# Optimization experiments

Hardware: AMD Instinct MI355X
Metric: run time of the kernel (lower is better)

The kernel has to match this reference:

```python
import jax, jax.numpy as jnp
import numpy as np

N = 100000   # every_node
IN = 128     # in_channels
OUT = 128    # out_channels
R = 8        # every_relation
B = 4        # num_bases
E = 1_600_000  # total edges (avg degree 16)
E_PER = E // R
LEAKY_SLOPE = 0.2


def _xavier_uniform(key, shape, gain):
    fan_in, fan_out = shape[-2], shape[-1]
    bound = gain * np.sqrt(6.0 / (fan_in + fan_out))
    return jax.random.uniform(key, shape, jnp.float32, -bound, bound)


def setup_inputs() -> dict:
    key = jax.random.key(0)
    k = jax.random.split(key, 6)
    gain = float(np.sqrt(2.0))  # calculate_gain('relu')
    node_embeddings = jax.random.normal(k[0], (N, IN), jnp.float32)
    src = jax.random.randint(k[1], (E,), 0, N, jnp.int32)
    dst = jax.random.randint(k[2], (E,), 0, N, jnp.int32)
    rel = jnp.repeat(jnp.arange(R, dtype=jnp.int32), E_PER)  # sorted by relation
    triples = jnp.stack([src, rel, dst], axis=1)  # [E,3] = (src, rel, dst)
    change_points = jnp.arange(0, E + 1, E_PER, dtype=jnp.int32)  # [R+1]
    basis = _xavier_uniform(k[3], (B, IN, OUT), gain)
    att = _xavier_uniform(k[4], (R, B), gain)
    attention = _xavier_uniform(k[5], (R, 2 * OUT), gain)
    bias = jnp.zeros((OUT,), jnp.float32)
    return {
        'node_embeddings': node_embeddings,
        'triples': triples,
        'change_points': change_points,
        'basis': basis,
        'att': att,
        'attention': attention,
        'bias': bias,
    }


def reference(node_embeddings, triples, change_points, basis, att, attention, bias):
    # Basis decomposition: per-relation weight, then per-relation transformed features.
    weights = jnp.einsum('rb,bio->rio', att, basis)              # [R, in, out]
    Wh = jnp.einsum('rio,ni->rno', weights, node_embeddings)     # [R, N, out]

    src, rel, dst = triples[:, 0], triples[:, 2], None  # placeholder; see below
    src = triples[:, 0]
    rel = triples[:, 1]   # triples are sorted by relation; rel column == block id from change_points
    dst = triples[:, 2]

    # Attention score a . [Wh_src || Wh_dst] decomposed into per-node partial scores.
    a_src = attention[:, :OUT]                                   # [R, out]
    a_dst = attention[:, OUT:]                                   # [R, out]
    s_src = jnp.einsum('rno,ro->rn', Wh, a_src)                  # [R, N]
    s_dst = jnp.einsum('rno,ro->rn', Wh, a_dst)                  # [R, N]
    e_raw = jax.nn.leaky_relu(s_src[rel, src] + s_dst[rel, dst], LEAKY_SLOPE)  # [E]

    # Segment softmax per (relation, dst) — matches per-relation scatter amax/add.
    seg = rel.astype(jnp.int32) * N + dst.astype(jnp.int32)
    e_max = jax.ops.segment_max(e_raw, seg, num_segments=R * N)
    e_exp = jnp.exp(e_raw - e_max[seg])
    denom = jax.ops.segment_sum(e_exp, seg, num_segments=R * N)
    alpha = e_exp / jnp.maximum(denom[seg], 1e-8)                # [E]
    # (attn dropout omitted: eval mode)

    # SpMM aggregation: sum over relations of A_rel @ Wh_rel.
    msgs = alpha[:, None] * Wh[rel, src]                         # [E, out]
    h_prime = jax.ops.segment_sum(msgs, dst, num_segments=N)     # [N, out]

    output = h_prime + bias
    if node_embeddings.shape[-1] == OUT:
        output = output + node_embeddings  # residual
    return output
```

## Files before the change

kernel.cpp:

```cpp
#include <hip/hip_runtime.h>
#include <stdint.h>

#define NN 100000
#define DIM 128
#define RR 8
#define BB 4
#define EE 1600000
#define EPR 200000
#define SLOPE 0.2f
#define CAP 64
#define NCONV 12500
#define NBG 12504
#define NBE 6250

typedef __attribute__((ext_vector_type(8))) short short8;
typedef __attribute__((ext_vector_type(4))) float f32x4;

__device__ __forceinline__ unsigned short f2bf(float f) {
    unsigned u = __float_as_uint(f);
    unsigned r = (u + 0x7FFFu + ((u >> 16) & 1u)) >> 16;
    return (unsigned short)r;
}

__global__ __launch_bounds__(256) void k_pre(const float* __restrict__ x,
        unsigned* __restrict__ xb, int* __restrict__ cnt,
        const float* __restrict__ att, const float* __restrict__ basis,
        const float* __restrict__ attention, unsigned short* __restrict__ wt,
        unsigned short* __restrict__ w16b) {
    int bid = blockIdx.x;
    if (bid < NCONV) {
        size_t t = (size_t)bid * 256 + threadIdx.x;
        float4 v = *(const float4*)(x + t * 4);
        uint2 o;
        o.x = (unsigned)f2bf(v.x) | ((unsigned)f2bf(v.y) << 16);
        o.y = (unsigned)f2bf(v.z) | ((unsigned)f2bf(v.w) << 16);
        *(uint2*)(xb + t * 2) = o;
        if (t < NN) cnt[t] = 0;
    } else {
        int r = bid - NCONV;
        int i = threadIdx.x;
        if (i < DIM) {
            float a[BB];
#pragma unroll
            for (int b = 0; b < BB; ++b) a[b] = att[r * BB + b];
            const float* asrc = attention + r * 2 * DIM;
            const float* adst = asrc + DIM;
            float ws = 0.f, wd = 0.f;
            for (int o = 0; o < DIM; ++o) {
                float w = 0.f;
#pragma unroll
                for (int b = 0; b < BB; ++b) w += a[b] * basis[(b * DIM + i) * DIM + o];
                wt[(r * DIM + o) * DIM + i] = f2bf(w);
                ws += w * asrc[o];
                wd += w * adst[o];
            }
            w16b[r * DIM + i] = f2bf(ws);
            w16b[(RR + r) * DIM + i] = f2bf(wd);
        }
    }
}

__global__ __launch_bounds__(256) void k_score16(const unsigned short* __restrict__ w16b,
        const unsigned short* __restrict__ xb, float* __restrict__ ssrc,
        float* __restrict__ sdst) {
    __shared__ unsigned short lw[16 * 136];
    for (int u = threadIdx.x; u < 16 * 16; u += 256) {
        int row = u >> 4, ch = u & 15;
        *(uint4*)&lw[row * 136 + ch * 8] = *(const uint4*)&w16b[row * 128 + ch * 8];
    }
    __syncthreads();
    int wave = threadIdx.x >> 6, lane = threadIdx.x & 63;
    int ncol = blockIdx.x * 64 + wave * 16 + (lane & 15);
    int nc = ncol < NN ? ncol : NN - 1;
    int kg = (lane >> 4) * 8;
    const short8* xrow = (const short8*)(xb + (size_t)nc * DIM);
    f32x4 acc = (f32x4){0.f, 0.f, 0.f, 0.f};
#pragma unroll
    for (int k = 0; k < 4; ++k) {
        short8 a = *(const short8*)&lw[(lane & 15) * 136 + k * 32 + kg];
        short8 b = xrow[k * 4 + (lane >> 4)];
        acc = __builtin_amdgcn_mfma_f32_16x16x32_bf16(a, b, acc, 0, 0, 0);
    }
    if (ncol < NN) {
#pragma unroll
        for (int j = 0; j < 4; ++j) {
            int row = (lane >> 4) * 4 + j;
            if (row < RR) ssrc[row * NN + ncol] = acc[j];
            else sdst[(row - RR) * NN + ncol] = acc[j];
        }
    }
}

__global__ __launch_bounds__(256) void k_main(const unsigned short* __restrict__ wt,
        const unsigned short* __restrict__ xb, unsigned short* __restrict__ wh,
        const int* __restrict__ tri, const float* __restrict__ ssrc,
        const float* __restrict__ sdst, int* __restrict__ cnt,
        unsigned* __restrict__ bucket) {
    __shared__ unsigned short lds[DIM * 136];
    int bid = blockIdx.x;
    if (bid < NBG) {
        int r = bid & 7;
        int ncol0 = (bid >> 3) * 64;
        {
            const uint4* src = (const uint4*)(wt + r * DIM * DIM);
            for (int u = threadIdx.x; u < DIM * DIM / 8; u += 256) {
                int row = u >> 4, ch = u & 15;
                *(uint4*)&lds[row * 136 + ch * 8] = src[u];
            }
        }
        __syncthreads();
        int wave = threadIdx.x >> 6, lane = threadIdx.x & 63;
        int ncol = ncol0 + wave * 16 + (lane & 15);
        int kg = (lane >> 4) * 8;
        int nc = ncol < NN ? ncol : NN - 1;
        const short8* xrow = (const short8*)(xb + (size_t)nc * DIM);
        short8 bfrag[4];
#pragma unroll
        for (int k = 0; k < 4; ++k) bfrag[k] = xrow[k * 4 + (lane >> 4)];
        f32x4 acc[8];
#pragma unroll
        for (int f = 0; f < 8; ++f) acc[f] = (f32x4){0.f, 0.f, 0.f, 0.f};
#pragma unroll
        for (int k = 0; k < 4; ++k) {
#pragma unroll
            for (int f = 0; f < 8; ++f) {
                short8 a = *(const short8*)&lds[(f * 16 + (lane & 15)) * 136 + k * 32 + kg];
                acc[f] = __builtin_amdgcn_mfma_f32_16x16x32_bf16(a, bfrag[k], acc[f], 0, 0, 0);
            }
        }
        __syncthreads();
        int lr = wave * 16 + (lane & 15);
        int cg = (lane >> 4) * 4;
#pragma unroll
        for (int f = 0; f < 8; ++f) {
            uint2 v;
            v.x = (unsigned)f2bf(acc[f][0]) | ((unsigned)f2bf(acc[f][1]) << 16);
            v.y = (unsigned)f2bf(acc[f][2]) | ((unsigned)f2bf(acc[f][3]) << 16);
            *(uint2*)&lds[lr * 132 + f * 16 + cg] = v;
        }
        __syncthreads();
        for (int it = 0; it < 4; ++it) {
            int idx = it * 256 + threadIdx.x;
            int row = idx >> 4, ch = idx & 15;
            int n = ncol0 + row;
            if (n < NN) {
                *(uint4*)&wh[((size_t)r * NN + n) * DIM + ch * 8] =
                    *(const uint4*)&lds[row * 132 + ch * 8];
            }
        }
    } else {
        int e = (bid - NBG) * 256 + threadIdx.x;
        int src = tri[3 * e], dst = tri[3 * e + 2];
        int rel = e / EPR;
        float er = ssrc[rel * NN + src] + sdst[rel * NN + dst];
        er = er > 0.f ? er : SLOPE * er;
        int q = (int)fmaf(er, 64.f, 2048.5f);
        q = q < 0 ? 0 : (q > 4095 ? 4095 : q);
        int pos = atomicAdd(&cnt[dst], 1);
        if (pos < CAP)
            bucket[(size_t)dst * CAP + pos] =
                (unsigned)src | ((unsigned)rel << 17) | ((unsigned)q << 20);
    }
}

__global__ __launch_bounds__(256, 8) void k_agg(const int* __restrict__ cnt,
        const unsigned* __restrict__ bucket, const unsigned* __restrict__ whu,
        const float* __restrict__ x, const float* __restrict__ bias,
        float* __restrict__ out) {
    int tid = threadIdx.x;
    int wave = tid >> 6, lane = tid & 63;
    int d = blockIdx.x * 4 + wave;
    int c = min(cnt[d], CAP);
    unsigned mv = 0;
    if (lane < c) mv = bucket[(size_t)d * CAP + lane];
    int rel = (int)((mv >> 17) & 7);
    float pl = (lane < c) ? __expf(fmaf((float)(mv >> 20), 0.015625f, -32.0f)) : 0.f;
    float sd[RR];
#pragma unroll
    for (int r = 0; r < RR; ++r) {
        float t = (rel == r) ? pl : 0.f;
#pragma unroll
        for (int o = 32; o > 0; o >>= 1) t += __shfl_xor(t, o);
        sd[r] = t;
    }
    float s = sd[0];
#pragma unroll
    for (int r = 1; r < RR; ++r) s = (rel == r) ? sd[r] : s;
    float al = pl * __builtin_amdgcn_rcpf(fmaxf(s, 1e-8f));

    float a0 = 0.f, a1 = 0.f;
    for (int j0 = 0; j0 < c; j0 += 8) {
        unsigned w[8];
        float av[8];
#pragma unroll
        for (int u = 0; u < 8; ++u) {
            unsigned mx = (unsigned)__shfl((int)mv, j0 + u);
            av[u] = __shfl(al, j0 + u);
            int row = (int)((mx >> 17) & 7) * NN + (int)(mx & 0x1FFFF);
            w[u] = whu[(size_t)row * 64 + lane];
        }
#pragma unroll
        for (int u = 0; u < 8; ++u) {
            a0 = fmaf(av[u], __uint_as_float(w[u] << 16), a0);
            a1 = fmaf(av[u], __uint_as_float(w[u] & 0xFFFF0000u), a1);
        }
    }
    float2 xv = *(const float2*)(x + (size_t)d * DIM + lane * 2);
    float2 bv = *(const float2*)(bias + lane * 2);
    float2 ov;
    ov.x = a0 + xv.x + bv.x;
    ov.y = a1 + xv.y + bv.y;
    *(float2*)(out + (size_t)d * DIM + lane * 2) = ov;
}

extern "C" void kernel_launch(void* const* d_in, const int* in_sizes, int n_in,
                              void* d_out, int out_size, void* d_ws, size_t ws_size,
                              hipStream_t stream) {
    const float* x = (const float*)d_in[0];
    const int* tri = (const int*)d_in[1];
    const float* basis = (const float*)d_in[3];
    const float* att = (const float*)d_in[4];
    const float* attention = (const float*)d_in[5];
    const float* bias = (const float*)d_in[6];
    float* out = (float*)d_out;

    char* ws = (char*)d_ws;
    size_t off = 0;
    auto alloc = [&](size_t b) {
        char* p = ws + off;
        off = (off + b + 255) & ~(size_t)255;
        return p;
    };
    unsigned short* wh = (unsigned short*)alloc((size_t)RR * NN * DIM * 2);
    unsigned* xb = (unsigned*)alloc((size_t)NN * DIM * 2);
    unsigned short* wt = (unsigned short*)alloc((size_t)RR * DIM * DIM * 2);
    unsigned short* w16b = (unsigned short*)alloc((size_t)16 * DIM * 2);
    float* ssrc = (float*)alloc((size_t)RR * NN * 4);
    float* sdst = (float*)alloc((size_t)RR * NN * 4);
    int* cnt = (int*)alloc((size_t)NN * 4);
    unsigned* bucket = (unsigned*)alloc((size_t)NN * CAP * 4);

    k_pre<<<NCONV + RR, 256, 0, stream>>>(x, xb, cnt, att, basis, attention, wt, w16b);
    k_score16<<<(NN + 63) / 64, 256, 0, stream>>>(w16b, (const unsigned short*)xb,
                                                  ssrc, sdst);
    k_main<<<NBG + NBE, 256, 0, stream>>>(wt, (const unsigned short*)xb, wh,
                                          tri, ssrc, sdst, cnt, bucket);
    k_agg<<<NN / 4, 256, 0, stream>>>(cnt, bucket, (const unsigned*)wh, x, bias, out);
}
```

Baseline: 278.2 us.

## XOR-swizzle weight LDS layout and precompute softmax denominators with atomics

Weights are now written pre-swizzled (16-byte chunk index XORed with row mod 8), so the GEMM block can copy them into an unpadded LDS tile and read MFMA fragments without bank conflicts, dropping the padded layout. Separately, the edge-scoring blocks accumulate per-(dst, relation) softmax denominators with float atomics into a new zero-initialized buffer. The aggregation kernel then reads the denominator directly instead of doing eight wave-wide shuffle reductions. This adds 1.6M scattered float atomics and an 800K-element zeroing pass in exchange for less shuffle work in aggregation. It also sums edges past CAP that aggregation drops.

Result: slower. 335.7 us (median of 3 runs) (+20.7%).

```diff
diff --git a/kernel.cpp b/kernel.cpp
--- a/kernel.cpp
+++ b/kernel.cpp
@@ -23,7 +23,7 @@
 }
 
 __global__ __launch_bounds__(256) void k_pre(const float* __restrict__ x,
-        unsigned* __restrict__ xb, int* __restrict__ cnt,
+        unsigned* __restrict__ xb, int* __restrict__ cnt, float* __restrict__ denom,
         const float* __restrict__ att, const float* __restrict__ basis,
         const float* __restrict__ attention, unsigned short* __restrict__ wt,
         unsigned short* __restrict__ w16b) {
@@ -36,6 +36,7 @@
         o.y = (unsigned)f2bf(v.z) | ((unsigned)f2bf(v.w) << 16);
         *(uint2*)(xb + t * 2) = o;
         if (t < NN) cnt[t] = 0;
+        if (t < (size_t)NN * RR) denom[t] = 0.f;
     } else {
         int r = bid - NCONV;
         int i = threadIdx.x;
@@ -45,12 +46,13 @@
             for (int b = 0; b < BB; ++b) a[b] = att[r * BB + b];
             const float* asrc = attention + r * 2 * DIM;
             const float* adst = asrc + DIM;
+            int gi = i >> 3, ii = i & 7;
             float ws = 0.f, wd = 0.f;
             for (int o = 0; o < DIM; ++o) {
                 float w = 0.f;
 #pragma unroll
                 for (int b = 0; b < BB; ++b) w += a[b] * basis[(b * DIM + i) * DIM + o];
-                wt[(r * DIM + o) * DIM + i] = f2bf(w);
+                wt[(r * DIM + o) * DIM + ((gi ^ (o & 7)) << 3) + ii] = f2bf(w);
                 ws += w * asrc[o];
                 wd += w * adst[o];
             }
@@ -95,28 +97,27 @@
         const unsigned short* __restrict__ xb, unsigned short* __restrict__ wh,
         const int* __restrict__ tri, const float* __restrict__ ssrc,
         const float* __restrict__ sdst, int* __restrict__ cnt,
-        unsigned* __restrict__ bucket) {
-    __shared__ unsigned short lds[DIM * 136];
+        unsigned* __restrict__ bucket, float* __restrict__ denom) {
+    __shared__ unsigned short lds[DIM * DIM];
     int bid = blockIdx.x;
     if (bid < NBG) {
         int r = bid & 7;
         int ncol0 = (bid >> 3) * 64;
         {
             const uint4* src = (const uint4*)(wt + r * DIM * DIM);
-            for (int u = threadIdx.x; u < DIM * DIM / 8; u += 256) {
-                int row = u >> 4, ch = u & 15;
-                *(uint4*)&lds[row * 136 + ch * 8] = src[u];
-            }
+            uint4* dstp = (uint4*)lds;
+            for (int u = threadIdx.x; u < DIM * DIM / 8; u += 256) dstp[u] = src[u];
         }
         __syncthreads();
         int wave = threadIdx.x >> 6, lane = threadIdx.x & 63;
-        int ncol = ncol0 + wave * 16 + (lane & 15);
-        int kg = (lane >> 4) * 8;
+        int m0 = lane & 15, gq = lane >> 4;
+        int key = m0 & 7;
+        int ncol = ncol0 + wave * 16 + m0;
         int nc = ncol < NN ? ncol : NN - 1;
         const short8* xrow = (const short8*)(xb + (size_t)nc * DIM);
         short8 bfrag[4];
 #pragma unroll
-        for (int k = 0; k < 4; ++k) bfrag[k] = xrow[k * 4 + (lane >> 4)];
+        for (int k = 0; k < 4; ++k) bfrag[k] = xrow[k * 4 + gq];
         f32x4 acc[8];
 #pragma unroll
         for (int f = 0; f < 8; ++f) acc[f] = (f32x4){0.f, 0.f, 0.f, 0.f};
@@ -124,13 +125,14 @@
         for (int k = 0; k < 4; ++k) {
 #pragma unroll
             for (int f = 0; f < 8; ++f) {
-                short8 a = *(const short8*)&lds[(f * 16 + (lane & 15)) * 136 + k * 32 + kg];
+                short8 a = *(const short8*)((const char*)lds +
+                          (size_t)(f * 16 + m0) * 256 + (((k * 4 + gq) ^ key) << 4));
                 acc[f] = __builtin_amdgcn_mfma_f32_16x16x32_bf16(a, bfrag[k], acc[f], 0, 0, 0);
             }
         }
         __syncthreads();
-        int lr = wave * 16 + (lane & 15);
-        int cg = (lane >> 4) * 4;
+        int lr = wave * 16 + m0;
+        int cg = gq * 4;
 #pragma unroll
         for (int f = 0; f < 8; ++f) {
             uint2 v;
@@ -156,6 +158,8 @@
         er = er > 0.f ? er : SLOPE * er;
         int q = (int)fmaf(er, 64.f, 2048.5f);
         q = q < 0 ? 0 : (q > 4095 ? 4095 : q);
+        float p = __expf(fmaf((float)q, 0.015625f, -32.0f));
+        atomicAdd(&denom[dst * RR + rel], p);
         int pos = atomicAdd(&cnt[dst], 1);
         if (pos < CAP)
             bucket[(size_t)dst * CAP + pos] =
@@ -164,9 +168,9 @@
 }
 
 __global__ __launch_bounds__(256, 8) void k_agg(const int* __restrict__ cnt,
-        const unsigned* __restrict__ bucket, const unsigned* __restrict__ whu,
-        const float* __restrict__ x, const float* __restrict__ bias,
-        float* __restrict__ out) {
+        const unsigned* __restrict__ bucket, const float* __restrict__ denom,
+        const unsigned* __restrict__ whu, const float* __restrict__ x,
+        const float* __restrict__ bias, float* __restrict__ out) {
     int tid = threadIdx.x;
     int wave = tid >> 6, lane = tid & 63;
     int d = blockIdx.x * 4 + wave;
@@ -175,17 +179,7 @@
     if (lane < c) mv = bucket[(size_t)d * CAP + lane];
     int rel = (int)((mv >> 17) & 7);
     float pl = (lane < c) ? __expf(fmaf((float)(mv >> 20), 0.015625f, -32.0f)) : 0.f;
-    float sd[RR];
-#pragma unroll
-    for (int r = 0; r < RR; ++r) {
-        float t = (rel == r) ? pl : 0.f;
-#pragma unroll
-        for (int o = 32; o > 0; o >>= 1) t += __shfl_xor(t, o);
-        sd[r] = t;
-    }
-    float s = sd[0];
-#pragma unroll
-    for (int r = 1; r < RR; ++r) s = (rel == r) ? sd[r] : s;
+    float s = denom[d * RR + rel];
     float al = pl * __builtin_amdgcn_rcpf(fmaxf(s, 1e-8f));
 
     float a0 = 0.f, a1 = 0.f;
@@ -237,13 +231,16 @@
     unsigned short* w16b = (unsigned short*)alloc((size_t)16 * DIM * 2);
     float* ssrc = (float*)alloc((size_t)RR * NN * 4);
     float* sdst = (float*)alloc((size_t)RR * NN * 4);
+    float* denom = (float*)alloc((size_t)NN * RR * 4);
     int* cnt = (int*)alloc((size_t)NN * 4);
     unsigned* bucket = (unsigned*)alloc((size_t)NN * CAP * 4);
 
-    k_pre<<<NCONV + RR, 256, 0, stream>>>(x, xb, cnt, att, basis, attention, wt, w16b);
+    k_pre<<<NCONV + RR, 256, 0, stream>>>(x, xb, cnt, denom, att, basis, attention,
+                                          wt, w16b);
     k_score16<<<(NN + 63) / 64, 256, 0, stream>>>(w16b, (const unsigned short*)xb,
                                                   ssrc, sdst);
     k_main<<<NBG + NBE, 256, 0, stream>>>(wt, (const unsigned short*)xb, wh,
-                                          tri, ssrc, sdst, cnt, bucket);
-    k_agg<<<NN / 4, 256, 0, stream>>>(cnt, bucket, (const unsigned*)wh, x, bias, out);
-}
+                                          tri, ssrc, sdst, cnt, bucket, denom);
+    k_agg<<<NN / 4, 256, 0, stream>>>(cnt, bucket, denom, (const unsigned*)wh, x,
+                                      bias, out);
+}
```
